# Kernel optimization log

Hardware: AMD Instinct MI355X
Metric: run time of the kernel (lower is better)

## Reference

```python
import jax, jax.numpy as jnp
import numpy as np

N = 100000      # nodes
E = 1600000     # edges (avg degree 16)
D_IN = 64
D_OUT = 64
EPS = 1e-9


def setup_inputs() -> dict:
    key = jax.random.key(0)
    ks = jax.random.split(key, 12)
    x = jax.random.normal(ks[0], (N, D_IN), dtype=jnp.float32)
    edge_row = jax.random.randint(ks[1], (E,), 0, N, dtype=jnp.int32)
    edge_col = jax.random.randint(ks[2], (E,), 0, N, dtype=jnp.int32)
    # positive normalized adjacency values (~1/degree scale)
    edge_val = jax.random.uniform(ks[3], (E,), dtype=jnp.float32) / 16.0
    lim = float(np.sqrt(6.0 / (D_IN + D_OUT)))  # xavier_uniform
    W0 = jax.random.uniform(ks[4], (D_OUT, D_IN), jnp.float32, -lim, lim)
    W1 = jax.random.uniform(ks[5], (D_OUT, D_IN), jnp.float32, -lim, lim)
    b0 = jnp.zeros((D_OUT,), jnp.float32)
    b1 = jnp.zeros((D_OUT,), jnp.float32)
    scale0 = jnp.ones((D_OUT,), jnp.float32)
    scale1 = jnp.ones((D_OUT,), jnp.float32)
    offset0 = jnp.zeros((D_OUT,), jnp.float32)
    offset1 = jnp.zeros((D_OUT,), jnp.float32)
    return {"x": x, "edge_val": edge_val, "W0": W0, "b0": b0,
            "scale0": scale0, "offset0": offset0, "W1": W1, "b1": b1,
            "scale1": scale1, "offset1": offset1,
            "edge_row": edge_row, "edge_col": edge_col}


def _hop_transform(feat, W, b, scale, offset):
    # Linear (no bias in nn.Linear) + separate bias + ReLU
    h = jax.nn.relu(feat @ W.T + b)                      # [N, D_OUT]
    # custom per-row normalization ('norm' branch)
    mean = jnp.mean(h, axis=1, keepdims=True)
    var = jnp.var(h, axis=1, keepdims=True) + EPS        # unbiased=False
    return (h - mean) * scale * jax.lax.rsqrt(var) + offset


def reference(x, edge_val, W0, b0, scale0, offset0, W1, b1, scale1, offset1,
              edge_row, edge_col):
    # SpMM: out[r] = sum_{e: row[e]==r} val[e] * x[col[e]]
    msgs = edge_val[:, None] * x[edge_col]               # [E, D_IN]
    agg = jax.ops.segment_sum(msgs, edge_row, num_segments=N)
    # order=1: hop-0 uses raw features, hop-1 uses aggregated features
    h0 = _hop_transform(x, W0, b0, scale0, offset0)
    h1 = _hop_transform(agg, W1, b1, scale1, offset1)
    # aggr='mean' -> elementwise sum of partial features
    return h0 + h1
```

## Files before the change

kernel.cpp:

```cpp
#include <hip/hip_runtime.h>

#define NN 100000
#define NE 1600000
#define DD 64
#define NB   391
#define NBK1 782
#define BCAP 4608
#define RCAP 40
#define NK3  1563

__device__ __forceinline__ unsigned short f2bfu(float f) {
    union { float f; unsigned u; } c; c.f = f;
    unsigned lsb = (c.u >> 16) & 1u;
    c.u += 0x7FFFu + lsb;
    return (unsigned short)(c.u >> 16);
}

typedef short v8s __attribute__((ext_vector_type(8)));
typedef float v4f __attribute__((ext_vector_type(4)));

__global__ __launch_bounds__(256) void init_kernel(
    const float* __restrict__ W0, const float* __restrict__ W1,
    int* __restrict__ gbcur,
    unsigned short* __restrict__ wb0, unsigned short* __restrict__ wb1)
{
    int i = blockIdx.x * 256 + threadIdx.x;
    if (i < NB) gbcur[i] = 0;
    if (i < DD * DD) { wb0[i] = f2bfu(W0[i]); wb1[i] = f2bfu(W1[i]); }
}

__global__ __launch_bounds__(256) void x2bf_kernel(
    const float* __restrict__ x, unsigned short* __restrict__ xb)
{
    int i = (blockIdx.x * 256 + threadIdx.x) * 8;
    float4 a = *(const float4*)(x + i);
    float4 b = *(const float4*)(x + i + 4);
    uint4 o;
    o.x = (unsigned)f2bfu(a.x) | ((unsigned)f2bfu(a.y) << 16);
    o.y = (unsigned)f2bfu(a.z) | ((unsigned)f2bfu(a.w) << 16);
    o.z = (unsigned)f2bfu(b.x) | ((unsigned)f2bfu(b.y) << 16);
    o.w = (unsigned)f2bfu(b.z) | ((unsigned)f2bfu(b.w) << 16);
    *(uint4*)(xb + i) = o;
}

__global__ __launch_bounds__(512) void bin_scatter_kernel(
    const int* __restrict__ row, const int* __restrict__ col,
    const float* __restrict__ val, int* __restrict__ gbcur,
    int2* __restrict__ bslab)
{
    __shared__ int2 rbuf[2048];
    __shared__ unsigned short bkts[2048];
    __shared__ int pscan[512];
    __shared__ int cnt[NB];
    __shared__ int pst[NB];
    __shared__ int cur[NB];
    __shared__ int gbase[NB];

    int b = blockIdx.x, t = threadIdx.x;
    int e = b * 2048 + t * 4;
    bool ok = (e + 3 < NE);

    for (int i = t; i < NB; i += 512) cnt[i] = 0;
    __syncthreads();

    int4 r, c; float4 v;
    if (ok) {
        r = *(const int4*)(row + e);
        c = *(const int4*)(col + e);
        v = *(const float4*)(val + e);
        atomicAdd(&cnt[r.x >> 8], 1);
        atomicAdd(&cnt[r.y >> 8], 1);
        atomicAdd(&cnt[r.z >> 8], 1);
        atomicAdd(&cnt[r.w >> 8], 1);
    }
    __syncthreads();
    pscan[t] = (t < NB) ? cnt[t] : 0;
    __syncthreads();
    for (int off = 1; off < 512; off <<= 1) {
        int u = (t >= off) ? pscan[t - off] : 0;
        __syncthreads();
        pscan[t] += u;
        __syncthreads();
    }
    if (t < NB) {
        int st = pscan[t] - cnt[t];
        pst[t] = st;
        cur[t] = st;
        gbase[t] = cnt[t] ? atomicAdd(&gbcur[t], cnt[t]) : 0;
    }
    __syncthreads();
    if (ok) {
        int bk, pos;
        bk = r.x >> 8; pos = atomicAdd(&cur[bk], 1);
        rbuf[pos] = make_int2(c.x | ((r.x & 255) << 17), __float_as_int(v.x));
        bkts[pos] = (unsigned short)bk;
        bk = r.y >> 8; pos = atomicAdd(&cur[bk], 1);
        rbuf[pos] = make_int2(c.y | ((r.y & 255) << 17), __float_as_int(v.y));
        bkts[pos] = (unsigned short)bk;
        bk = r.z >> 8; pos = atomicAdd(&cur[bk], 1);
        rbuf[pos] = make_int2(c.z | ((r.z & 255) << 17), __float_as_int(v.z));
        bkts[pos] = (unsigned short)bk;
        bk = r.w >> 8; pos = atomicAdd(&cur[bk], 1);
        rbuf[pos] = make_int2(c.w | ((r.w & 255) << 17), __float_as_int(v.w));
        bkts[pos] = (unsigned short)bk;
    }
    __syncthreads();
    int ntot = pscan[511];
    for (int i = t; i < ntot; i += 512) {
        int bk = bkts[i];
        int gi = gbase[bk] + (i - pst[bk]);
        if (gi < BCAP) bslab[(size_t)bk * BCAP + gi] = rbuf[i];
    }
}

#define BF4FMA(G, VV, ACC) { \
    ACC.x = fmaf(VV, __uint_as_float((G).x << 16), ACC.x); \
    ACC.y = fmaf(VV, __uint_as_float((G).x & 0xFFFF0000u), ACC.y); \
    ACC.z = fmaf(VV, __uint_as_float((G).y << 16), ACC.z); \
    ACC.w = fmaf(VV, __uint_as_float((G).y & 0xFFFF0000u), ACC.w); }

__global__ __launch_bounds__(256, 5) void sort_pull_mfma_kernel(
    const unsigned short* __restrict__ xb, const int* __restrict__ gbcur,
    const int2* __restrict__ bslab,
    const unsigned short* __restrict__ wb0, const unsigned short* __restrict__ wb1,
    const float* __restrict__ b0, const float* __restrict__ s0, const float* __restrict__ o0,
    const float* __restrict__ b1, const float* __restrict__ s1, const float* __restrict__ o1,
    float* __restrict__ out)
{
    __shared__ int2 ebuf[64][RCAP];
    __shared__ unsigned aggt[4][16][36];
    __shared__ int cur[64];

    int phys = blockIdx.x;
    int xc = phys & 7, ii = phys >> 3;
    int p = (xc < 3) ? xc * 196 + ii : 588 + (xc - 3) * 195 + ii;

    int t = threadIdx.x, lane = t & 63, wv = t >> 6;
    int sub = lane & 15, q = lane >> 4;
    int bkt = p >> 2, quarter = p & 3;
    int nb = min(gbcur[bkt], BCAP);
    const int2* bp = bslab + (size_t)bkt * BCAP;

    if (t < 64) cur[t] = 0;
    __syncthreads();
    for (int i = t; i < nb; i += 256) {
        int2 rc = bp[i];
        int rl = (rc.x >> 17) & 255;
        if ((rl >> 6) == quarter) {
            int pos = atomicAdd(&cur[rl & 63], 1);
            if (pos < RCAP) ebuf[rl & 63][pos] = make_int2(rc.x & 0x1FFFF, rc.y);
        }
    }
    __syncthreads();

    int nb0 = p * 64 + wv * 16;
    if (nb0 < NN) {
        for (int rr = 0; rr < 16; ++rr) {
            int lr = wv * 16 + rr;
            int d = min(cur[lr], RCAP);
            int cc = (d + 7) >> 3;
            int plen = cc * 8;
            if (lane < plen - d) ebuf[lr][d + lane] = make_int2(0, 0);

            float4 acc = make_float4(0.f, 0.f, 0.f, 0.f);
            int ch = 0;
            for (; ch + 2 <= cc; ch += 2) {
                int2 r0 = ebuf[lr][ch * 8 + q];
                int2 r1 = ebuf[lr][ch * 8 + 4 + q];
                int2 r2 = ebuf[lr][ch * 8 + 8 + q];
                int2 r3 = ebuf[lr][ch * 8 + 12 + q];
                uint2 g0 = *(const uint2*)(xb + (size_t)r0.x * DD + sub * 4);
                uint2 g1 = *(const uint2*)(xb + (size_t)r1.x * DD + sub * 4);
                uint2 g2 = *(const uint2*)(xb + (size_t)r2.x * DD + sub * 4);
                uint2 g3 = *(const uint2*)(xb + (size_t)r3.x * DD + sub * 4);
                float v0 = __int_as_float(r0.y), v1 = __int_as_float(r1.y);
                float v2 = __int_as_float(r2.y), v3 = __int_as_float(r3.y);
                BF4FMA(g0, v0, acc); BF4FMA(g1, v1, acc);
                BF4FMA(g2, v2, acc); BF4FMA(g3, v3, acc);
            }
            if (ch < cc) {
                int2 r0 = ebuf[lr][ch * 8 + q];
                int2 r1 = ebuf[lr][ch * 8 + 4 + q];
                uint2 g0 = *(const uint2*)(xb + (size_t)r0.x * DD + sub * 4);
                uint2 g1 = *(const uint2*)(xb + (size_t)r1.x * DD + sub * 4);
                float v0 = __int_as_float(r0.y), v1 = __int_as_float(r1.y);
                BF4FMA(g0, v0, acc); BF4FMA(g1, v1, acc);
            }
            acc.x += __shfl_xor(acc.x, 16, 64); acc.y += __shfl_xor(acc.y, 16, 64);
            acc.z += __shfl_xor(acc.z, 16, 64); acc.w += __shfl_xor(acc.w, 16, 64);
            acc.x += __shfl_xor(acc.x, 32, 64); acc.y += __shfl_xor(acc.y, 32, 64);
            acc.z += __shfl_xor(acc.z, 32, 64); acc.w += __shfl_xor(acc.w, 32, 64);
            if (q == 0) {
                uint2 pk;
                pk.x = (unsigned)f2bfu(acc.x) | ((unsigned)f2bfu(acc.y) << 16);
                pk.y = (unsigned)f2bfu(acc.z) | ((unsigned)f2bfu(acc.w) << 16);
                *(uint2*)&aggt[wv][rr][sub * 2] = pk;
            }
        }

        v8s ax[2], aa[2];
#pragma unroll
        for (int ks = 0; ks < 2; ++ks) {
            ax[ks] = *(const v8s*)(xb + (size_t)(nb0 + sub) * DD + ks * 32 + q * 8);
            aa[ks] = *(const v8s*)&aggt[wv][sub][ks * 16 + q * 4];
        }

        float h0v[4][4], h1v[4][4];
        float sr0[4] = {0,0,0,0}, sq0[4] = {0,0,0,0};
        float sr1[4] = {0,0,0,0}, sq1[4] = {0,0,0,0};
#pragma unroll
        for (int dt = 0; dt < 4; ++dt) {
            int nidx = dt * 16 + sub;
            float bi0 = b0[nidx], bi1 = b1[nidx];
            v8s w00 = *(const v8s*)(wb0 + nidx * 64 + q * 8);
            v8s w01 = *(const v8s*)(wb0 + nidx * 64 + 32 + q * 8);
            v8s w10 = *(const v8s*)(wb1 + nidx * 64 + q * 8);
            v8s w11 = *(const v8s*)(wb1 + nidx * 64 + 32 + q * 8);
            v4f c0 = (v4f){bi0, bi0, bi0, bi0};
            v4f c1 = (v4f){bi1, bi1, bi1, bi1};
            c0 = __builtin_amdgcn_mfma_f32_16x16x32_bf16(ax[0], w00, c0, 0, 0, 0);
            c0 = __builtin_amdgcn_mfma_f32_16x16x32_bf16(ax[1], w01, c0, 0, 0, 0);
            c1 = __builtin_amdgcn_mfma_f32_16x16x32_bf16(aa[0], w10, c1, 0, 0, 0);
            c1 = __builtin_amdgcn_mfma_f32_16x16x32_bf16(aa[1], w11, c1, 0, 0, 0);
#pragma unroll
            for (int r = 0; r < 4; ++r) {
                float h = fmaxf(c0[r], 0.f); h0v[dt][r] = h; sr0[r] += h; sq0[r] += h * h;
                float g = fmaxf(c1[r], 0.f); h1v[dt][r] = g; sr1[r] += g; sq1[r] += g * g;
            }
        }
#pragma unroll
        for (int off = 1; off < 16; off <<= 1) {
#pragma unroll
            for (int r = 0; r < 4; ++r) {
                sr0[r] += __shfl_xor(sr0[r], off, 64);
                sq0[r] += __shfl_xor(sq0[r], off, 64);
                sr1[r] += __shfl_xor(sr1[r], off, 64);
                sq1[r] += __shfl_xor(sq1[r], off, 64);
            }
        }

        float scl0[4], scl1[4], ofs0[4], ofs1[4];
#pragma unroll
        for (int dt = 0; dt < 4; ++dt) {
            int nidx = dt * 16 + sub;
            scl0[dt] = s0[nidx]; scl1[dt] = s1[nidx];
            ofs0[dt] = o0[nidx]; ofs1[dt] = o1[nidx];
        }

        const float inv = 1.0f / 64.0f;
#pragma unroll
        for (int r = 0; r < 4; ++r) {
            float m0 = sr0[r] * inv;
            float v0 = fmaxf(sq0[r] * inv - m0 * m0, 0.f) + 1e-9f;
            float m1 = sr1[r] * inv;
            float v1 = fmaxf(sq1[r] * inv - m1 * m1, 0.f) + 1e-9f;
            float rs0 = rsqrtf(v0), rs1 = rsqrtf(v1);
            int node = nb0 + q * 4 + r;
#pragma unroll
            for (int dt = 0; dt < 4; ++dt) {
                float rv = (h0v[dt][r] - m0) * scl0[dt] * rs0 + ofs0[dt]
                         + (h1v[dt][r] - m1) * scl1[dt] * rs1 + ofs1[dt];
                out[(size_t)node * DD + dt * 16 + sub] = rv;
            }
        }
    }
}

extern "C" void kernel_launch(void* const* d_in, const int* in_sizes, int n_in,
                              void* d_out, int out_size, void* d_ws, size_t ws_size,
                              hipStream_t stream) {
    const float* x  = (const float*)d_in[0];
    const float* ev = (const float*)d_in[1];
    const float* W0 = (const float*)d_in[2];
    const float* b0 = (const float*)d_in[3];
    const float* s0 = (const float*)d_in[4];
    const float* o0 = (const float*)d_in[5];
    const float* W1 = (const float*)d_in[6];
    const float* b1 = (const float*)d_in[7];
    const float* s1 = (const float*)d_in[8];
    const float* o1 = (const float*)d_in[9];
    const int* row = (const int*)d_in[10];
    const int* col = (const int*)d_in[11];

    char* wsb = (char*)d_ws;
    int*  gbcur = (int*)wsb;
    unsigned short* wb0 = (unsigned short*)(wsb + 1600);
    unsigned short* wb1 = (unsigned short*)(wsb + 9792);
    unsigned short* xb = (unsigned short*)(wsb + 18048);
    int2* bslab = (int2*)(wsb + 12818048);

    init_kernel<<<16, 256, 0, stream>>>(W0, W1, gbcur, wb0, wb1);
    x2bf_kernel<<<3125, 256, 0, stream>>>(x, xb);
    bin_scatter_kernel<<<NBK1, 512, 0, stream>>>(row, col, ev, gbcur, bslab);
    sort_pull_mfma_kernel<<<NK3, 256, 0, stream>>>(
        xb, gbcur, bslab, wb0, wb1, b0, s0, o0, b1, s1, o1, (float*)d_out);
}
```

Baseline: 201.3 us.

## Merge prep kernels, double edges per scatter block, reuse ebuf LDS for aggregates

```diff
diff --git a/kernel.cpp b/kernel.cpp
--- a/kernel.cpp
+++ b/kernel.cpp
@@ -4,7 +4,7 @@
 #define NE 1600000
 #define DD 64
 #define NB   391
-#define NBK1 782
+#define NBK1 391
 #define BCAP 4608
 #define RCAP 40
 #define NK3  1563
@@ -19,20 +19,19 @@
 typedef short v8s __attribute__((ext_vector_type(8)));
 typedef float v4f __attribute__((ext_vector_type(4)));
 
-__global__ __launch_bounds__(256) void init_kernel(
-    const float* __restrict__ W0, const float* __restrict__ W1,
+__global__ __launch_bounds__(256) void prep_kernel(
+    const float* __restrict__ x, const float* __restrict__ W0,
+    const float* __restrict__ W1, unsigned short* __restrict__ xb,
     int* __restrict__ gbcur,
     unsigned short* __restrict__ wb0, unsigned short* __restrict__ wb1)
 {
-    int i = blockIdx.x * 256 + threadIdx.x;
-    if (i < NB) gbcur[i] = 0;
-    if (i < DD * DD) { wb0[i] = f2bfu(W0[i]); wb1[i] = f2bfu(W1[i]); }
-}
-
-__global__ __launch_bounds__(256) void x2bf_kernel(
-    const float* __restrict__ x, unsigned short* __restrict__ xb)
-{
-    int i = (blockIdx.x * 256 + threadIdx.x) * 8;
+    int t = threadIdx.x, blk = blockIdx.x;
+    if (blk < 16) {
+        int j = blk * 256 + t;
+        if (j < NB) gbcur[j] = 0;
+        if (j < DD * DD) { wb0[j] = f2bfu(W0[j]); wb1[j] = f2bfu(W1[j]); }
+    }
+    int i = (blk * 256 + t) * 8;
     float4 a = *(const float4*)(x + i);
     float4 b = *(const float4*)(x + i + 4);
     uint4 o;
@@ -48,8 +47,8 @@
     const float* __restrict__ val, int* __restrict__ gbcur,
     int2* __restrict__ bslab)
 {
-    __shared__ int2 rbuf[2048];
-    __shared__ unsigned short bkts[2048];
+    __shared__ int2 rbuf[4096];
+    __shared__ unsigned short bkts[4096];
     __shared__ int pscan[512];
     __shared__ int cnt[NB];
     __shared__ int pst[NB];
@@ -57,21 +56,25 @@
     __shared__ int gbase[NB];
 
     int b = blockIdx.x, t = threadIdx.x;
-    int e = b * 2048 + t * 4;
-    bool ok = (e + 3 < NE);
+    int e0 = b * 4096;
 
     for (int i = t; i < NB; i += 512) cnt[i] = 0;
     __syncthreads();
 
-    int4 r, c; float4 v;
-    if (ok) {
-        r = *(const int4*)(row + e);
-        c = *(const int4*)(col + e);
-        v = *(const float4*)(val + e);
-        atomicAdd(&cnt[r.x >> 8], 1);
-        atomicAdd(&cnt[r.y >> 8], 1);
-        atomicAdd(&cnt[r.z >> 8], 1);
-        atomicAdd(&cnt[r.w >> 8], 1);
+    int4 r[2], c[2]; float4 v[2]; bool ok[2];
+#pragma unroll
+    for (int h = 0; h < 2; ++h) {
+        int e = e0 + t * 8 + h * 4;
+        ok[h] = (e + 3 < NE);
+        if (ok[h]) {
+            r[h] = *(const int4*)(row + e);
+            c[h] = *(const int4*)(col + e);
+            v[h] = *(const float4*)(val + e);
+            atomicAdd(&cnt[r[h].x >> 8], 1);
+            atomicAdd(&cnt[r[h].y >> 8], 1);
+            atomicAdd(&cnt[r[h].z >> 8], 1);
+            atomicAdd(&cnt[r[h].w >> 8], 1);
+        }
     }
     __syncthreads();
     pscan[t] = (t < NB) ? cnt[t] : 0;
@@ -89,20 +92,23 @@
         gbase[t] = cnt[t] ? atomicAdd(&gbcur[t], cnt[t]) : 0;
     }
     __syncthreads();
-    if (ok) {
-        int bk, pos;
-        bk = r.x >> 8; pos = atomicAdd(&cur[bk], 1);
-        rbuf[pos] = make_int2(c.x | ((r.x & 255) << 17), __float_as_int(v.x));
-        bkts[pos] = (unsigned short)bk;
-        bk = r.y >> 8; pos = atomicAdd(&cur[bk], 1);
-        rbuf[pos] = make_int2(c.y | ((r.y & 255) << 17), __float_as_int(v.y));
-        bkts[pos] = (unsigned short)bk;
-        bk = r.z >> 8; pos = atomicAdd(&cur[bk], 1);
-        rbuf[pos] = make_int2(c.z | ((r.z & 255) << 17), __float_as_int(v.z));
-        bkts[pos] = (unsigned short)bk;
-        bk = r.w >> 8; pos = atomicAdd(&cur[bk], 1);
-        rbuf[pos] = make_int2(c.w | ((r.w & 255) << 17), __float_as_int(v.w));
-        bkts[pos] = (unsigned short)bk;
+#pragma unroll
+    for (int h = 0; h < 2; ++h) {
+        if (ok[h]) {
+            int bk, pos;
+            bk = r[h].x >> 8; pos = atomicAdd(&cur[bk], 1);
+            rbuf[pos] = make_int2(c[h].x | ((r[h].x & 255) << 17), __float_as_int(v[h].x));
+            bkts[pos] = (unsigned short)bk;
+            bk = r[h].y >> 8; pos = atomicAdd(&cur[bk], 1);
+            rbuf[pos] = make_int2(c[h].y | ((r[h].y & 255) << 17), __float_as_int(v[h].y));
+            bkts[pos] = (unsigned short)bk;
+            bk = r[h].z >> 8; pos = atomicAdd(&cur[bk], 1);
+            rbuf[pos] = make_int2(c[h].z | ((r[h].z & 255) << 17), __float_as_int(v[h].z));
+            bkts[pos] = (unsigned short)bk;
+            bk = r[h].w >> 8; pos = atomicAdd(&cur[bk], 1);
+            rbuf[pos] = make_int2(c[h].w | ((r[h].w & 255) << 17), __float_as_int(v[h].w));
+            bkts[pos] = (unsigned short)bk;
+        }
     }
     __syncthreads();
     int ntot = pscan[511];
@@ -119,7 +125,7 @@
     ACC.z = fmaf(VV, __uint_as_float((G).y << 16), ACC.z); \
     ACC.w = fmaf(VV, __uint_as_float((G).y & 0xFFFF0000u), ACC.w); }
 
-__global__ __launch_bounds__(256, 5) void sort_pull_mfma_kernel(
+__global__ __launch_bounds__(256, 7) void sort_pull_mfma_kernel(
     const unsigned short* __restrict__ xb, const int* __restrict__ gbcur,
     const int2* __restrict__ bslab,
     const unsigned short* __restrict__ wb0, const unsigned short* __restrict__ wb1,
@@ -128,7 +134,6 @@
     float* __restrict__ out)
 {
     __shared__ int2 ebuf[64][RCAP];
-    __shared__ unsigned aggt[4][16][36];
     __shared__ int cur[64];
 
     int phys = blockIdx.x;
@@ -194,7 +199,7 @@
                 uint2 pk;
                 pk.x = (unsigned)f2bfu(acc.x) | ((unsigned)f2bfu(acc.y) << 16);
                 pk.y = (unsigned)f2bfu(acc.z) | ((unsigned)f2bfu(acc.w) << 16);
-                *(uint2*)&aggt[wv][rr][sub * 2] = pk;
+                *(uint2*)&(((unsigned*)&ebuf[lr][0])[sub * 2]) = pk;
             }
         }
 
@@ -202,7 +207,7 @@
 #pragma unroll
         for (int ks = 0; ks < 2; ++ks) {
             ax[ks] = *(const v8s*)(xb + (size_t)(nb0 + sub) * DD + ks * 32 + q * 8);
-            aa[ks] = *(const v8s*)&aggt[wv][sub][ks * 16 + q * 4];
+            aa[ks] = *(const v8s*)&(((unsigned*)&ebuf[wv * 16 + sub][0])[ks * 16 + q * 4]);
         }
 
         float h0v[4][4], h1v[4][4];
@@ -289,8 +294,7 @@
     unsigned short* xb = (unsigned short*)(wsb + 18048);
     int2* bslab = (int2*)(wsb + 12818048);
 
-    init_kernel<<<16, 256, 0, stream>>>(W0, W1, gbcur, wb0, wb1);
-    x2bf_kernel<<<3125, 256, 0, stream>>>(x, xb);
+    prep_kernel<<<3125, 256, 0, stream>>>(x, W0, W1, xb, gbcur, wb0, wb1);
     bin_scatter_kernel<<<NBK1, 512, 0, stream>>>(row, col, ev, gbcur, bslab);
     sort_pull_mfma_kernel<<<NK3, 256, 0, stream>>>(
         xb, gbcur, bslab, wb0, wb1, b0, s0, o0, b1, s1, o1, (float*)d_out);
```

Measured after the change: 175.0 us. 13.1% less time.
